# Kernel optimization log

Hardware: AMD Instinct MI355X
Metric: run time of the kernel (lower is better)

The kernel has to match this reference:

```python
import jax, jax.numpy as jnp
import numpy as np

N = 50000      # num_nodes
R = 90         # num_relations
E = 800000     # num_edges
H = 16         # hidden channels
B = 30         # num_bases
C = 8          # num_classes


def setup_inputs() -> dict:
    key = jax.random.key(0)
    ks = jax.random.split(key, 10)
    edge_index = jax.random.randint(ks[0], (2, E), 0, N, dtype=jnp.int64)
    edge_type = jax.random.randint(ks[1], (E,), 0, R, dtype=jnp.int64)
    s1 = 1.0 / np.sqrt(N)
    s2 = 1.0 / np.sqrt(H)
    return {
        "edge_index": edge_index,
        "edge_type": edge_type,
        # layer 1: in=N (featureless one-hot), out=H
        "basis1": jax.random.normal(ks[2], (B, N, H), jnp.float32) * s1,
        "comp1": jax.random.normal(ks[3], (R, B), jnp.float32) * (1.0 / np.sqrt(B)),
        "root1": jax.random.normal(ks[4], (N, H), jnp.float32) * s1,
        "bias1": jnp.zeros((H,), jnp.float32),
        # layer 2: in=H, out=C
        "basis2": jax.random.normal(ks[5], (B, H, C), jnp.float32) * s2,
        "comp2": jax.random.normal(ks[6], (R, B), jnp.float32) * (1.0 / np.sqrt(B)),
        "root2": jax.random.normal(ks[7], (H, C), jnp.float32) * s2,
        "bias2": jnp.zeros((C,), jnp.float32),
    }


def reference(edge_index, edge_type, basis1, comp1, root1, bias1,
              basis2, comp2, root2, bias2):
    src, dst = edge_index[0], edge_index[1]
    # per-(dst, relation) degree -> mean aggregation per relation (PyG RGCNConv aggr='mean')
    seg = dst * R + edge_type                      # [E]
    deg = jax.ops.segment_sum(jnp.ones((E,), jnp.float32), seg, num_segments=N * R)
    inv_deg = jnp.where(deg > 0, 1.0 / jnp.maximum(deg, 1.0), 0.0)
    norm = inv_deg[seg][:, None]                   # [E, 1]

    # ---- layer 1 (x = None -> one-hot node features; message = W_r[src]) ----
    W1 = jnp.einsum('rb,bnh->rnh', comp1, basis1)  # [R, N, H]
    m1 = W1[edge_type, src] * norm                 # [E, H]
    h = jax.ops.segment_sum(m1, dst, num_segments=N) + root1 + bias1  # [N, H]
    h = jax.nn.relu(h)

    # ---- layer 2 ----
    W2 = jnp.einsum('rb,bhc->rhc', comp2, basis2)  # [R, H, C]
    m2 = jnp.einsum('eh,ehc->ec', h[src], W2[edge_type]) * norm       # [E, C]
    out = jax.ops.segment_sum(m2, dst, num_segments=N) + h @ root2 + bias2
    return jax.nn.log_softmax(out, axis=1)
```

## Files before the change

kernel.cpp:

```cpp
#include <hip/hip_runtime.h>

#define NNODES 50000
#define NREL   90
#define NEDGE  800000
#define HDIM   16
#define NBASIS 30
#define NCLS   8
#define NPART  392
#define CH     4096
#define P1BLK  ((NEDGE + CH - 1) / CH)
#define CAPSTG 2816
#define GS     8
#define BSTR2  260
#define CROW2  20

typedef __fp16 h2 __attribute__((ext_vector_type(2)));

static __device__ __forceinline__ unsigned pk2(float a, float b) {
    h2 p = __builtin_amdgcn_cvt_pkrtz(a, b);
    return __builtin_bit_cast(unsigned, p);
}
static __device__ __forceinline__ h2 uph(unsigned u) {
    return __builtin_bit_cast(h2, u);
}
static __device__ __forceinline__ float fd2(unsigned a, unsigned b, float c) {
#if __has_builtin(__builtin_amdgcn_fdot2)
    return __builtin_amdgcn_fdot2(uph(a), uph(b), c, false);
#else
    h2 x = uph(a), y = uph(b);
    return fmaf((float)x.y, (float)y.y, fmaf((float)x.x, (float)y.x, c));
#endif
}

__device__ __forceinline__ void scan512_incl(int* sc) {
    int t = threadIdx.x;
#pragma unroll
    for (int d = 1; d < 512; d <<= 1) {
        int v0 = sc[t];
        int a0 = (t >= d) ? sc[t - d] : 0;
        int v1 = sc[t + 256];
        int a1 = sc[t + 256 - d];
        __syncthreads();
        sc[t] = v0 + a0;
        sc[t + 256] = v1 + a1;
        __syncthreads();
    }
}

__device__ __forceinline__ void scan128_incl(int* sc) {
    int t = threadIdx.x;
#pragma unroll
    for (int d = 1; d < 128; d <<= 1) {
        int v = 0, a = 0;
        if (t < 128) { v = sc[t]; a = (t >= d) ? sc[t - d] : 0; }
        __syncthreads();
        if (t < 128) sc[t] = v + a;
        __syncthreads();
    }
}

__global__ __launch_bounds__(256) void initc_kernel(int* __restrict__ gcur_s,
                                                    int* __restrict__ gcur_d,
                                                    int* __restrict__ gcnt,
                                                    const float* __restrict__ comp1,
                                                    unsigned* __restrict__ comp_pk) {
    int t = blockIdx.x * 256 + threadIdx.x;
    if (t < NPART) { gcur_s[t] = t * CAPSTG; gcur_d[t] = t * CAPSTG; }
    else if (t == NPART) { gcnt[0] = 0; gcnt[1] = 0; }
    int i = t - 512;
    if (i >= 0 && i < NREL * 15) {
        int r = i / 15;
        int b2 = i - r * 15;
        comp_pk[r * CROW2 + b2] = pk2(comp1[r * NBASIS + 2 * b2],
                                      comp1[r * NBASIS + 2 * b2 + 1]);
    }
    if (i >= NREL * 15 && i < NREL * 15 + NREL * (CROW2 - 15)) {
        int j = i - NREL * 15;
        int r = j / (CROW2 - 15);
        int pcol = 15 + (j - r * (CROW2 - 15));
        comp_pk[r * CROW2 + pcol] = 0;
    }
}

__global__ __launch_bounds__(256) void p1d_kernel(const int* __restrict__ ei,
                                                  const int* __restrict__ et,
                                                  int* __restrict__ gcur_d,
                                                  int2* __restrict__ stg_d) {
    __shared__ int2 sorted[CH];
    __shared__ int hist[NPART], loff[NPART], cur[NPART], gbase[NPART];
    __shared__ int sc[512];
    int base = blockIdx.x * CH;
    int nitems = min(CH, NEDGE - base);
    int t = threadIdx.x;
    for (int i = t; i < NPART; i += 256) hist[i] = 0;
    __syncthreads();
    for (int i = t; i < nitems; i += 256)
        atomicAdd(&hist[ei[NEDGE + base + i] >> 7], 1);
    __syncthreads();
    sc[t]       = (t < NPART) ? hist[t] : 0;
    sc[t + 256] = (t + 256 < NPART) ? hist[t + 256] : 0;
    __syncthreads();
    scan512_incl(sc);
    for (int p = t; p < NPART; p += 256) {
        int lo = p ? sc[p - 1] : 0;
        loff[p] = lo;
        cur[p] = lo;
        if (hist[p]) gbase[p] = atomicAdd(&gcur_d[p], hist[p]);
    }
    __syncthreads();
    for (int i = t; i < nitems; i += 256) {
        int e = base + i;
        int src = ei[e], dst = ei[NEDGE + e], r = et[e];
        int rk = atomicAdd(&cur[dst >> 7], 1);
        sorted[rk] = make_int2(src | (r << 16), dst);
    }
    __syncthreads();
    for (int s = t; s < nitems; s += 256) {
        int2 it = sorted[s];
        int p = it.y >> 7;
        stg_d[gbase[p] + (s - loff[p])] = it;
    }
}

__global__ __launch_bounds__(256) void p2d_kernel(const int* __restrict__ gcur_d,
                                                  const int2* __restrict__ stg_d,
                                                  int* __restrict__ gcur_s,
                                                  int2* __restrict__ stg_s,
                                                  int* __restrict__ gcnt,
                                                  int* __restrict__ d_sr,
                                                  float* __restrict__ d_norm,
                                                  int* __restrict__ offs_d,
                                                  int* __restrict__ cnt_d) {
    __shared__ int2 sorted[CAPSTG];
    __shared__ int2 sorted2[CAPSTG];
    __shared__ int h[128], off[128], cur[128];
    __shared__ int sc[512];
    __shared__ int shist[NPART], sloff[NPART], scur[NPART], sgbase[NPART];
    __shared__ int kb;
    int p = blockIdx.x;
    int base = p * CAPSTG;
    int n = min(gcur_d[p] - base, CAPSTG);
    int t = threadIdx.x;
    if (t < 128) h[t] = 0;
    __syncthreads();
    for (int s = t; s < n; s += 256)
        atomicAdd(&h[stg_d[base + s].y & 127], 1);
    __syncthreads();
    if (t < 128) sc[t] = h[t];
    __syncthreads();
    scan128_incl(sc);
    if (t < 128) { int lo = t ? sc[t - 1] : 0; off[t] = lo; cur[t] = lo; }
    if (t == 0) kb = atomicAdd(&gcnt[0], n);
    __syncthreads();
    for (int s = t; s < n; s += 256) {
        int2 it = stg_d[base + s];
        int rk = atomicAdd(&cur[it.y & 127], 1);
        sorted[rk] = it;
    }
    __syncthreads();
    int kbase = kb;
    for (int s = t; s < n; s += 256) {
        int2 it = sorted[s];
        int key = it.y & 127;
        int r = it.x >> 16;
        int o = off[key], oe = o + h[key];
        int c = 0;
        for (int kk = o; kk < oe; ++kk)
            c += ((sorted[kk].x >> 16) == r);
        d_sr[kbase + s] = it.x;
        d_norm[kbase + s] = 1.0f / (float)c;
    }
    if (t < 128) {
        int node = (p << 7) + t;
        if (node < NNODES) { offs_d[node] = kbase + off[t]; cnt_d[node] = h[t]; }
    }
    for (int i = t; i < NPART; i += 256) shist[i] = 0;
    __syncthreads();
    for (int s = t; s < n; s += 256)
        atomicAdd(&shist[(sorted[s].x & 0xFFFF) >> 7], 1);
    __syncthreads();
    sc[t]       = (t < NPART) ? shist[t] : 0;
    sc[t + 256] = (t + 256 < NPART) ? shist[t + 256] : 0;
    __syncthreads();
    scan512_incl(sc);
    for (int pp = t; pp < NPART; pp += 256) {
        int lo = pp ? sc[pp - 1] : 0;
        sloff[pp] = lo;
        scur[pp] = lo;
        if (shist[pp]) sgbase[pp] = atomicAdd(&gcur_s[pp], shist[pp]);
    }
    __syncthreads();
    for (int s = t; s < n; s += 256) {
        int2 it = sorted[s];
        int rk = atomicAdd(&scur[(it.x & 0xFFFF) >> 7], 1);
        sorted2[rk] = make_int2(it.x, kbase + s);
    }
    __syncthreads();
    for (int s = t; s < n; s += 256) {
        int2 it = sorted2[s];
        int pp = (it.x & 0xFFFF) >> 7;
        stg_s[sgbase[pp] + (s - sloff[pp])] = it;
    }
}

__global__ __launch_bounds__(256) void p2s_kernel(const int* __restrict__ gcur_s,
                                                  const int2* __restrict__ stg_s,
                                                  int* __restrict__ gcnt,
                                                  int* __restrict__ sB,
                                                  int* __restrict__ s_k,
                                                  int* __restrict__ offs_s,
                                                  int* __restrict__ cnt_s) {
    __shared__ int2 sorted[CAPSTG];
    __shared__ int h[128], off[128], cur[128], sc[128];
    __shared__ int jb;
    int p = blockIdx.x;
    int base = p * CAPSTG;
    int n = min(gcur_s[p] - base, CAPSTG);
    int t = threadIdx.x;
    if (t < 128) h[t] = 0;
    __syncthreads();
    for (int s = t; s < n; s += 256)
        atomicAdd(&h[stg_s[base + s].x & 127], 1);
    __syncthreads();
    if (t < 128) sc[t] = h[t];
    __syncthreads();
    scan128_incl(sc);
    if (t < 128) { int lo = t ? sc[t - 1] : 0; off[t] = lo; cur[t] = lo; }
    if (t == 0) jb = atomicAdd(&gcnt[1], n);
    __syncthreads();
    for (int s = t; s < n; s += 256) {
        int2 it = stg_s[base + s];
        int rk = atomicAdd(&cur[it.x & 127], 1);
        sorted[rk] = it;
    }
    __syncthreads();
    int jbase = jb;
    for (int s = t; s < n; s += 256) {
        int2 it = sorted[s];
        sB[jbase + s]  = it.x;
        s_k[jbase + s] = it.y;
    }
    if (t < 128) {
        int node = (p << 7) + t;
        if (node < NNODES) { offs_s[node] = jbase + off[t]; cnt_s[node] = h[t]; }
    }
}

__global__ __launch_bounds__(256) void msg1_lds(const float* __restrict__ basis1,
                                                const unsigned* __restrict__ comp_pk,
                                                const int* __restrict__ offs_s,
                                                const int* __restrict__ cnt_s,
                                                const int* __restrict__ sB,
                                                const int* __restrict__ s_k,
                                                unsigned* __restrict__ m1) {
    __shared__ unsigned bspk[GS * BSTR2];
    __shared__ unsigned cpk[NREL * CROW2];
    int src0 = blockIdx.x * GS;
    int t = threadIdx.x;
    for (int i = t; i < NREL * CROW2; i += 256)
        cpk[i] = comp_pk[i];
    for (int i4 = t; i4 < 15 * 32; i4 += 256) {
        int b2 = i4 >> 5;
        int w  = i4 & 31;
        const float4* bp = (const float4*)basis1;
        float4 a = bp[(size_t)(2 * b2)     * (NNODES * 4) + (size_t)src0 * 4 + w];
        float4 b = bp[(size_t)(2 * b2 + 1) * (NNODES * 4) + (size_t)src0 * 4 + w];
        int s = w >> 2, q = w & 3;
        uint4 o;
        o.x = pk2(a.x, b.x);
        o.y = pk2(a.y, b.y);
        o.z = pk2(a.z, b.z);
        o.w = pk2(a.w, b.w);
        *((uint4*)(bspk + s * BSTR2 + b2 * 16 + q * 4)) = o;
    }
    __syncthreads();
    int n0 = offs_s[src0];
    int lastS = src0 + GS - 1;
    int n1 = offs_s[lastS] + cnt_s[lastS];
    for (int ii = n0 * 4 + t; ii < n1 * 4; ii += 256) {
        int j = ii >> 2;
        int q = ii & 3;
        int pk = sB[j];
        int k  = s_k[j];
        int src = pk & 0xFFFF;
        int r   = pk >> 16;
        const uint4* crow = (const uint4*)(cpk + r * CROW2);
        uint4 c0 = crow[0], c1 = crow[1], c2 = crow[2], c3 = crow[3];
        const unsigned* bw = bspk + (src - src0) * BSTR2 + q * 4;
        float a0 = 0.f, a1 = 0.f, a2 = 0.f, a3 = 0.f;
#define MSG1_STEP(B2, CB) { \
        uint4 v = *((const uint4*)(bw + (B2) * 16)); \
        a0 = fd2(v.x, (CB), a0); \
        a1 = fd2(v.y, (CB), a1); \
        a2 = fd2(v.z, (CB), a2); \
        a3 = fd2(v.w, (CB), a3); }
        MSG1_STEP(0,  c0.x) MSG1_STEP(1,  c0.y) MSG1_STEP(2,  c0.z) MSG1_STEP(3,  c0.w)
        MSG1_STEP(4,  c1.x) MSG1_STEP(5,  c1.y) MSG1_STEP(6,  c1.z) MSG1_STEP(7,  c1.w)
        MSG1_STEP(8,  c2.x) MSG1_STEP(9,  c2.y) MSG1_STEP(10, c2.z) MSG1_STEP(11, c2.w)
        MSG1_STEP(12, c3.x) MSG1_STEP(13, c3.y) MSG1_STEP(14, c3.z)
#undef MSG1_STEP
        ((uint2*)m1)[(size_t)k * 4 + q] = make_uint2(pk2(a0, a1), pk2(a2, a3));
    }
}

__global__ __launch_bounds__(256) void gather1_flat(const unsigned* __restrict__ m1,
                                                    const float* __restrict__ d_norm,
                                                    const int* __restrict__ offs_d,
                                                    const int* __restrict__ cnt_d,
                                                    const float* __restrict__ root1,
                                                    const float* __restrict__ bias1,
                                                    float* __restrict__ h) {
    int idx = blockIdx.x * blockDim.x + threadIdx.x;
    if (idx >= NNODES * 4) return;
    int dst = idx >> 2;
    int q   = idx & 3;
    int k0 = offs_d[dst];
    int k1 = k0 + cnt_d[dst];
    float4 acc = make_float4(0.f, 0.f, 0.f, 0.f);
    for (int k = k0; k < k1; ++k) {
        uint2 v = ((const uint2*)m1)[(size_t)k * 4 + q];
        float nm = d_norm[k];
        h2 x = uph(v.x), y = uph(v.y);
        acc.x = fmaf(nm, (float)x.x, acc.x);
        acc.y = fmaf(nm, (float)x.y, acc.y);
        acc.z = fmaf(nm, (float)y.x, acc.z);
        acc.w = fmaf(nm, (float)y.y, acc.w);
    }
    float4 rt = ((const float4*)root1)[idx];
    float4 bi = ((const float4*)bias1)[q];
    float4 o;
    o.x = fmaxf(acc.x + rt.x + bi.x, 0.f);
    o.y = fmaxf(acc.y + rt.y + bi.y, 0.f);
    o.z = fmaxf(acc.z + rt.z + bi.z, 0.f);
    o.w = fmaxf(acc.w + rt.w + bi.w, 0.f);
    ((float4*)h)[idx] = o;
}

__global__ __launch_bounds__(256) void w2_kernel(const float* __restrict__ basis2,
                                                 const float* __restrict__ comp2,
                                                 const float* __restrict__ root2,
                                                 float* __restrict__ w2t,
                                                 float* __restrict__ r2t) {
    int i = blockIdx.x * blockDim.x + threadIdx.x;
    if (i >= NREL * HDIM * NCLS) return;
    int kk = i & (HDIM - 1);
    int c  = (i >> 4) & (NCLS - 1);
    int r  = i >> 7;
    float acc = 0.f;
#pragma unroll
    for (int b = 0; b < NBASIS; ++b)
        acc += comp2[r * NBASIS + b] * basis2[(b * HDIM + kk) * NCLS + c];
    w2t[i] = acc;
    if (i < HDIM * NCLS) {
        int c2 = i >> 4;
        int k2 = i & (HDIM - 1);
        r2t[i] = root2[k2 * NCLS + c2];
    }
}

__global__ __launch_bounds__(256) void msg2_kernel(const float* __restrict__ h,
                                                   const float* __restrict__ w2t,
                                                   const int* __restrict__ d_sr,
                                                   const float* __restrict__ d_norm,
                                                   float* __restrict__ m2) {
    int idx = blockIdx.x * blockDim.x + threadIdx.x;
    int k = idx >> 3;
    int c = idx & (NCLS - 1);
    int pk = d_sr[k];
    float nm = d_norm[k];
    int src = pk & 0xFFFF;
    int r   = pk >> 16;
    const float4* __restrict__ hp = (const float4*)h + src * 4;
    const float4* __restrict__ wp = (const float4*)w2t + (r * NCLS + c) * 4;
    float a = 0.f;
#pragma unroll
    for (int qq = 0; qq < 4; ++qq) {
        float4 hv = hp[qq];
        float4 wv = wp[qq];
        a = fmaf(hv.x, wv.x, a);
        a = fmaf(hv.y, wv.y, a);
        a = fmaf(hv.z, wv.z, a);
        a = fmaf(hv.w, wv.w, a);
    }
    m2[idx] = nm * a;
}

__global__ __launch_bounds__(256) void gather2_kernel(const float* __restrict__ m2,
                                                      const float* __restrict__ h,
                                                      const float* __restrict__ r2t,
                                                      const int* __restrict__ offs_d,
                                                      const int* __restrict__ cnt_d,
                                                      const float* __restrict__ bias2,
                                                      float* __restrict__ out) {
    int idx = blockIdx.x * blockDim.x + threadIdx.x;
    if (idx >= NNODES * NCLS) return;
    int dst = idx >> 3;
    int c   = idx & (NCLS - 1);
    int k0 = offs_d[dst];
    int k1 = k0 + cnt_d[dst];
    float acc = 0.f;
    for (int k = k0; k < k1; ++k)
        acc += m2[k * NCLS + c];
    float v = acc + bias2[c];
    const float4* __restrict__ hd = (const float4*)h + dst * 4;
    const float4* __restrict__ rp = (const float4*)r2t + c * 4;
#pragma unroll
    for (int qq = 0; qq < 4; ++qq) {
        float4 hv = hd[qq];
        float4 rv = rp[qq];
        v = fmaf(hv.x, rv.x, v);
        v = fmaf(hv.y, rv.y, v);
        v = fmaf(hv.z, rv.z, v);
        v = fmaf(hv.w, rv.w, v);
    }
    float mx = v;
    mx = fmaxf(mx, __shfl_xor(mx, 1));
    mx = fmaxf(mx, __shfl_xor(mx, 2));
    mx = fmaxf(mx, __shfl_xor(mx, 4));
    float s = expf(v - mx);
    s += __shfl_xor(s, 1);
    s += __shfl_xor(s, 2);
    s += __shfl_xor(s, 4);
    out[idx] = v - mx - logf(s);
}

__global__ __launch_bounds__(256) void degcnt_fb(const int* __restrict__ ei,
                                                 const int* __restrict__ et,
                                                 int* __restrict__ deg) {
    int e = blockIdx.x * blockDim.x + threadIdx.x;
    if (e >= NEDGE) return;
    atomicAdd(&deg[ei[NEDGE + e] * NREL + et[e]], 1);
}

__global__ __launch_bounds__(256) void layer1_flat(const int* __restrict__ ei,
                                                   const int* __restrict__ et,
                                                   const float* __restrict__ basis1,
                                                   const float* __restrict__ comp1,
                                                   const int* __restrict__ deg,
                                                   float* __restrict__ h) {
    long long idx = (long long)blockIdx.x * blockDim.x + threadIdx.x;
    if (idx >= (long long)NEDGE * HDIM) return;
    int e  = (int)(idx >> 4);
    int hh = (int)(idx & (HDIM - 1));
    int src = ei[e];
    int dst = ei[NEDGE + e];
    int r   = et[e];
    float norm = 1.0f / (float)deg[dst * NREL + r];
    const float* __restrict__ cp = comp1 + r * NBASIS;
    float acc = 0.f;
#pragma unroll
    for (int b = 0; b < NBASIS; ++b)
        acc += cp[b] * basis1[(b * NNODES + src) * HDIM + hh];
    atomicAdd(&h[dst * HDIM + hh], norm * acc);
}

__global__ __launch_bounds__(256) void relu_kernel(float* __restrict__ h,
                                                   const float* __restrict__ root1,
                                                   const float* __restrict__ bias1) {
    int i = blockIdx.x * blockDim.x + threadIdx.x;
    if (i >= NNODES * HDIM) return;
    float v = h[i] + root1[i] + bias1[i & (HDIM - 1)];
    h[i] = v > 0.f ? v : 0.f;
}

__global__ __launch_bounds__(256) void layer2_flat(const int* __restrict__ ei,
                                                   const int* __restrict__ et,
                                                   const float* __restrict__ h,
                                                   const float* __restrict__ w2t,
                                                   const int* __restrict__ deg,
                                                   float* __restrict__ out_tmp) {
    long long idx = (long long)blockIdx.x * blockDim.x + threadIdx.x;
    if (idx >= (long long)NEDGE * NCLS) return;
    int e = (int)(idx >> 3);
    int c = (int)(idx & (NCLS - 1));
    int src = ei[e];
    int dst = ei[NEDGE + e];
    int r   = et[e];
    float norm = 1.0f / (float)deg[dst * NREL + r];
    const float4* __restrict__ hp = (const float4*)h + src * 4;
    const float4* __restrict__ wp = (const float4*)w2t + (r * NCLS + c) * 4;
    float a = 0.f;
#pragma unroll
    for (int qq = 0; qq < 4; ++qq) {
        float4 hv = hp[qq];
        float4 wv = wp[qq];
        a = fmaf(hv.x, wv.x, a);
        a = fmaf(hv.y, wv.y, a);
        a = fmaf(hv.z, wv.z, a);
        a = fmaf(hv.w, wv.w, a);
    }
    atomicAdd(&out_tmp[dst * NCLS + c], norm * a);
}

__global__ __launch_bounds__(256) void final_kernel(const float* __restrict__ out_tmp,
                                                    const float* __restrict__ h,
                                                    const float* __restrict__ root2,
                                                    const float* __restrict__ bias2,
                                                    float* __restrict__ out) {
    int n = blockIdx.x * blockDim.x + threadIdx.x;
    if (n >= NNODES) return;
    float hv[HDIM];
#pragma unroll
    for (int i = 0; i < HDIM; ++i) hv[i] = h[n * HDIM + i];
    float v[NCLS];
    float mx = -1e30f;
#pragma unroll
    for (int c = 0; c < NCLS; ++c) {
        float acc = out_tmp[n * NCLS + c] + bias2[c];
#pragma unroll
        for (int i = 0; i < HDIM; ++i) acc += hv[i] * root2[i * NCLS + c];
        v[c] = acc;
        mx = fmaxf(mx, acc);
    }
    float s = 0.f;
#pragma unroll
    for (int c = 0; c < NCLS; ++c) s += expf(v[c] - mx);
    float ls = logf(s);
#pragma unroll
    for (int c = 0; c < NCLS; ++c) out[n * NCLS + c] = v[c] - mx - ls;
}

extern "C" void kernel_launch(void* const* d_in, const int* in_sizes, int n_in,
                              void* d_out, int out_size, void* d_ws, size_t ws_size,
                              hipStream_t stream) {
    const int*   ei     = (const int*)d_in[0];
    const int*   et     = (const int*)d_in[1];
    const float* basis1 = (const float*)d_in[2];
    const float* comp1  = (const float*)d_in[3];
    const float* root1  = (const float*)d_in[4];
    const float* bias1  = (const float*)d_in[5];
    const float* basis2 = (const float*)d_in[6];
    const float* comp2  = (const float*)d_in[7];
    const float* root2  = (const float*)d_in[8];
    const float* bias2  = (const float*)d_in[9];
    float* out = (float*)d_out;

    int*      gcur_s  = (int*)d_ws;
    int*      gcur_d  = gcur_s + NPART;
    int*      gcnt    = gcur_d + NPART;
    unsigned* comp_pk = (unsigned*)(gcnt + 4);
    int2*  stg_d  = (int2*)(comp_pk + NREL * CROW2);
    int2*  stg_s  = stg_d + (size_t)NPART * CAPSTG;
    int*   d_sr   = (int*)(stg_s + (size_t)NPART * CAPSTG);
    float* d_norm = (float*)(d_sr + NEDGE);
    int*   sB     = (int*)(d_norm + NEDGE);
    int*   s_k    = sB + NEDGE;
    int*   offs_s = s_k + NEDGE;
    int*   cnt_s  = offs_s + NNODES;
    int*   offs_d = cnt_s + NNODES;
    int*   cnt_d  = offs_d + NNODES;
    unsigned* m1  = (unsigned*)(cnt_d + NNODES);
    float* m2     = (float*)m1;
    float* h      = (float*)(m1 + (size_t)NEDGE * 8);
    float* w2t    = h + (size_t)NNODES * HDIM;
    float* r2t    = w2t + (size_t)NREL * HDIM * NCLS;
    size_t total_words = 2 * (size_t)NPART + 4 + NREL * CROW2 +
                         4 * (size_t)NPART * CAPSTG +
                         4 * (size_t)NEDGE + 4 * (size_t)NNODES +
                         (size_t)NEDGE * 8 + (size_t)NNODES * HDIM +
                         (size_t)NREL * HDIM * NCLS + HDIM * NCLS;

    if (ws_size >= total_words * sizeof(float)) {
        initc_kernel<<<8, 256, 0, stream>>>(gcur_s, gcur_d, gcnt, comp1, comp_pk);
        p1d_kernel<<<P1BLK, 256, 0, stream>>>(ei, et, gcur_d, stg_d);
        p2d_kernel<<<NPART - 1, 256, 0, stream>>>(gcur_d, stg_d, gcur_s, stg_s, gcnt,
                                                  d_sr, d_norm, offs_d, cnt_d);
        p2s_kernel<<<NPART - 1, 256, 0, stream>>>(gcur_s, stg_s, gcnt, sB, s_k, offs_s, cnt_s);

        msg1_lds<<<NNODES / GS, 256, 0, stream>>>(basis1, comp_pk, offs_s, cnt_s, sB, s_k, m1);
        gather1_flat<<<(NNODES * 4 + 255) / 256, 256, 0, stream>>>(
            m1, d_norm, offs_d, cnt_d, root1, bias1, h);
        w2_kernel<<<(NREL * HDIM * NCLS + 255) / 256, 256, 0, stream>>>(basis2, comp2, root2,
                                                                        w2t, r2t);
        msg2_kernel<<<(NEDGE * NCLS) / 256, 256, 0, stream>>>(h, w2t, d_sr, d_norm, m2);
        gather2_kernel<<<(NNODES * NCLS + 255) / 256, 256, 0, stream>>>(
            m2, h, r2t, offs_d, cnt_d, bias2, out);
        return;
    }

    {
        int*   deg_f   = (int*)d_ws;
        float* h_f     = (float*)(deg_f + (size_t)NNODES * NREL);
        float* out_tmp = h_f + (size_t)NNODES * HDIM;
        size_t zw = (size_t)NNODES * NREL + NNODES * HDIM + NNODES * NCLS;
        float* w2t_f   = out_tmp + (size_t)NNODES * NCLS;
        float* r2t_f   = w2t_f + (size_t)NREL * HDIM * NCLS;

        (void)hipMemsetAsync(d_ws, 0, zw * sizeof(float), stream);
        degcnt_fb<<<(NEDGE + 255) / 256, 256, 0, stream>>>(ei, et, deg_f);
        layer1_flat<<<((size_t)NEDGE * HDIM + 255) / 256, 256, 0, stream>>>(
            ei, et, basis1, comp1, deg_f, h_f);
        relu_kernel<<<(NNODES * HDIM + 255) / 256, 256, 0, stream>>>(h_f, root1, bias1);
        w2_kernel<<<(NREL * HDIM * NCLS + 255) / 256, 256, 0, stream>>>(basis2, comp2, root2,
                                                                        w2t_f, r2t_f);
        layer2_flat<<<((size_t)NEDGE * NCLS + 255) / 256, 256, 0, stream>>>(
            ei, et, h_f, w2t_f, deg_f, out_tmp);
        final_kernel<<<(NNODES + 255) / 256, 256, 0, stream>>>(out_tmp, h_f, root2, bias2, out);
    }
}
```

Measured before the change: 173.3 us.

## Fuse layer-2 message and gather into one wave-per-destination kernel

Replaces the separate msg2 and gather2 kernels with one kernel that assigns a wavefront to each destination node. Eight edge groups of eight class lanes compute messages on the fly and reduce them with shuffles, so the per-edge m2 buffer is never written or re-read. It also halves the partition chunk size CH and widens the comp_pk LDS load to uint4. The cost is idle lanes on low-degree nodes and more first-pass blocks from the smaller chunk.

```diff
diff --git a/kernel.cpp b/kernel.cpp
--- a/kernel.cpp
+++ b/kernel.cpp
@@ -7,7 +7,7 @@
 #define NBASIS 30
 #define NCLS   8
 #define NPART  392
-#define CH     4096
+#define CH     2048
 #define P1BLK  ((NEDGE + CH - 1) / CH)
 #define CAPSTG 2816
 #define GS     8
@@ -257,8 +257,8 @@
     __shared__ unsigned cpk[NREL * CROW2];
     int src0 = blockIdx.x * GS;
     int t = threadIdx.x;
-    for (int i = t; i < NREL * CROW2; i += 256)
-        cpk[i] = comp_pk[i];
+    for (int i = t; i < (NREL * CROW2) / 4; i += 256)
+        ((uint4*)cpk)[i] = ((const uint4*)comp_pk)[i];
     for (int i4 = t; i4 < 15 * 32; i4 += 256) {
         int b2 = i4 >> 5;
         int w  = i4 & 31;
@@ -358,51 +358,49 @@
     }
 }
 
-__global__ __launch_bounds__(256) void msg2_kernel(const float* __restrict__ h,
-                                                   const float* __restrict__ w2t,
-                                                   const int* __restrict__ d_sr,
-                                                   const float* __restrict__ d_norm,
-                                                   float* __restrict__ m2) {
-    int idx = blockIdx.x * blockDim.x + threadIdx.x;
-    int k = idx >> 3;
-    int c = idx & (NCLS - 1);
-    int pk = d_sr[k];
-    float nm = d_norm[k];
-    int src = pk & 0xFFFF;
-    int r   = pk >> 16;
-    const float4* __restrict__ hp = (const float4*)h + src * 4;
-    const float4* __restrict__ wp = (const float4*)w2t + (r * NCLS + c) * 4;
-    float a = 0.f;
-#pragma unroll
-    for (int qq = 0; qq < 4; ++qq) {
-        float4 hv = hp[qq];
-        float4 wv = wp[qq];
-        a = fmaf(hv.x, wv.x, a);
-        a = fmaf(hv.y, wv.y, a);
-        a = fmaf(hv.z, wv.z, a);
-        a = fmaf(hv.w, wv.w, a);
-    }
-    m2[idx] = nm * a;
-}
-
-__global__ __launch_bounds__(256) void gather2_kernel(const float* __restrict__ m2,
-                                                      const float* __restrict__ h,
-                                                      const float* __restrict__ r2t,
-                                                      const int* __restrict__ offs_d,
-                                                      const int* __restrict__ cnt_d,
-                                                      const float* __restrict__ bias2,
-                                                      float* __restrict__ out) {
-    int idx = blockIdx.x * blockDim.x + threadIdx.x;
-    if (idx >= NNODES * NCLS) return;
-    int dst = idx >> 3;
-    int c   = idx & (NCLS - 1);
+__global__ __launch_bounds__(256) void layer2_fused(const float* __restrict__ h,
+                                                    const float* __restrict__ w2t,
+                                                    const float* __restrict__ r2t,
+                                                    const int* __restrict__ offs_d,
+                                                    const int* __restrict__ cnt_d,
+                                                    const int* __restrict__ d_sr,
+                                                    const float* __restrict__ d_norm,
+                                                    const float* __restrict__ bias2,
+                                                    float* __restrict__ out) {
+    int wid  = threadIdx.x >> 6;
+    int lane = threadIdx.x & 63;
+    int dst  = blockIdx.x * 4 + wid;
+    int c = lane & (NCLS - 1);
+    int g = lane >> 3;
     int k0 = offs_d[dst];
     int k1 = k0 + cnt_d[dst];
+    const float4* __restrict__ h4 = (const float4*)h;
+    const float4* __restrict__ w4 = (const float4*)w2t;
     float acc = 0.f;
-    for (int k = k0; k < k1; ++k)
-        acc += m2[k * NCLS + c];
+    for (int k = k0 + g; k < k1; k += 8) {
+        int   pk = d_sr[k];
+        float nm = d_norm[k];
+        int src = pk & 0xFFFF;
+        int r   = pk >> 16;
+        const float4* __restrict__ hp = h4 + src * 4;
+        const float4* __restrict__ wp = w4 + (r * NCLS + c) * 4;
+        float a = 0.f;
+#pragma unroll
+        for (int qq = 0; qq < 4; ++qq) {
+            float4 hv = hp[qq];
+            float4 wv = wp[qq];
+            a = fmaf(hv.x, wv.x, a);
+            a = fmaf(hv.y, wv.y, a);
+            a = fmaf(hv.z, wv.z, a);
+            a = fmaf(hv.w, wv.w, a);
+        }
+        acc = fmaf(nm, a, acc);
+    }
+    acc += __shfl_xor(acc, 8);
+    acc += __shfl_xor(acc, 16);
+    acc += __shfl_xor(acc, 32);
     float v = acc + bias2[c];
-    const float4* __restrict__ hd = (const float4*)h + dst * 4;
+    const float4* __restrict__ hd = h4 + dst * 4;
     const float4* __restrict__ rp = (const float4*)r2t + c * 4;
 #pragma unroll
     for (int qq = 0; qq < 4; ++qq) {
@@ -421,7 +419,7 @@
     s += __shfl_xor(s, 1);
     s += __shfl_xor(s, 2);
     s += __shfl_xor(s, 4);
-    out[idx] = v - mx - logf(s);
+    if (g == 0) out[dst * NCLS + c] = v - mx - logf(s);
 }
 
 __global__ __launch_bounds__(256) void degcnt_fb(const int* __restrict__ ei,
@@ -550,7 +548,6 @@
     int*   offs_d = cnt_s + NNODES;
     int*   cnt_d  = offs_d + NNODES;
     unsigned* m1  = (unsigned*)(cnt_d + NNODES);
-    float* m2     = (float*)m1;
     float* h      = (float*)(m1 + (size_t)NEDGE * 8);
     float* w2t    = h + (size_t)NNODES * HDIM;
     float* r2t    = w2t + (size_t)NREL * HDIM * NCLS;
@@ -572,9 +569,8 @@
             m1, d_norm, offs_d, cnt_d, root1, bias1, h);
         w2_kernel<<<(NREL * HDIM * NCLS + 255) / 256, 256, 0, stream>>>(basis2, comp2, root2,
                                                                         w2t, r2t);
-        msg2_kernel<<<(NEDGE * NCLS) / 256, 256, 0, stream>>>(h, w2t, d_sr, d_norm, m2);
-        gather2_kernel<<<(NNODES * NCLS + 255) / 256, 256, 0, stream>>>(
-            m2, h, r2t, offs_d, cnt_d, bias2, out);
+        layer2_fused<<<NNODES / 4, 256, 0, stream>>>(h, w2t, r2t, offs_d, cnt_d,
+                                                     d_sr, d_norm, bias2, out);
         return;
     }
 
```

After: 179.4 us. +3.5%, slower.
